# Performance work log

Hardware: AMD Instinct MI355X
Metric: run time of the kernel (lower is better)

Reference implementation:

```python
import jax, jax.numpy as jnp
import numpy as np

N, E, H, NH = 50000, 800000, 128, 4
D = H // NH
EPS = 1e-5


def _ln(x, g, b):
    m = jnp.mean(x, axis=-1, keepdims=True)
    v = jnp.mean((x - m) ** 2, axis=-1, keepdims=True)
    return (x - m) * jax.lax.rsqrt(v + EPS) * g + b


def setup_inputs() -> dict:
    key = jax.random.key(0)
    ks = jax.random.split(key, 16)

    def lin(k, fi, fo):
        w = jax.random.normal(k, (fi, fo), jnp.float32) * (1.0 / np.sqrt(fi))
        return w, jnp.zeros((fo,), jnp.float32)

    h = jax.random.normal(ks[0], (N, H), jnp.float32)
    e = jax.random.normal(ks[1], (E, H), jnp.float32)
    src = jax.random.randint(ks[2], (E,), 0, N, jnp.int32)
    dst = jax.random.randint(ks[3], (E,), 0, N, jnp.int32)

    Wq, bq = lin(ks[4], H, H)
    Wk, bk = lin(ks[5], 2 * H, H)
    Wv, bv = lin(ks[6], 2 * H, H)
    Wn1, bn1 = lin(ks[7], H, H)
    Wn2, bn2 = lin(ks[8], H, H)
    We1, be1 = lin(ks[9], 3 * H, H)
    We2, be2 = lin(ks[10], H, H)
    gh = jnp.ones((H,), jnp.float32)
    bh = jnp.zeros((H,), jnp.float32)
    ge = jnp.ones((H,), jnp.float32)
    be = jnp.zeros((H,), jnp.float32)

    return dict(h=h, e=e, src=src, dst=dst, Wq=Wq, bq=bq, Wk=Wk, bk=bk,
                Wv=Wv, bv=bv, Wn1=Wn1, bn1=bn1, Wn2=Wn2, bn2=bn2,
                We1=We1, be1=be1, We2=We2, be2=be2, gh=gh, bh=bh, ge=ge, be=be)


def reference(h, e, src, dst, Wq, bq, Wk, bk, Wv, bv, Wn1, bn1, Wn2, bn2,
              We1, be1, We2, be2, gh, bh, ge, be):
    # gather src node features onto edges, concat with edge features: [E, 2H]
    m = jnp.concatenate([h[src], e], axis=-1)
    Q = (h @ Wq + bq).reshape(N, NH, D)
    K = (m @ Wk + bk).reshape(E, NH, D)
    V = (m @ Wv + bv).reshape(E, NH, D)

    # per-edge multihead attention score against destination query: [E, NH]
    s = jnp.sum(Q[dst] * K, axis=-1) / np.sqrt(D).astype(np.float32)

    # destination-grouped (segment) softmax per head
    smax = jax.ops.segment_max(s, dst, num_segments=N)  # [N, NH]
    a = jnp.exp(s - smax[dst])
    denom = jax.ops.segment_sum(a, dst, num_segments=N)  # [N, NH]
    a = a / denom[dst]

    # weighted scatter-sum of values back to destination nodes
    msg = V * a[..., None]  # [E, NH, D]
    h_agg = jax.ops.segment_sum(msg, dst, num_segments=N).reshape(N, H)

    # node MLP update (dropout = identity in eval) + residual + LayerNorm
    h_new = jax.nn.relu(jax.nn.relu(h_agg @ Wn1 + bn1) @ Wn2 + bn2)
    h_out = _ln(h + h_new, gh, bh)

    # edge MLP update on [src_h, dst_h, e] + residual + LayerNorm
    me = jnp.concatenate([h_out[src], h_out[dst], e], axis=-1)  # [E, 3H]
    e_new = jax.nn.relu(jax.nn.relu(me @ We1 + be1) @ We2 + be2)
    e_out = _ln(e + e_new, ge, be)
    return h_out, e_out
```

## Files before the change

### kernel.cpp

```cpp
#include <hip/hip_runtime.h>
#include <hip/hip_bf16.h>

#define NN 50000
#define EE 800000
#define HH 128

typedef __attribute__((ext_vector_type(8))) short bf16x8;
typedef __attribute__((ext_vector_type(4))) float f32x4;

__device__ inline unsigned short f2bf(float f) {
    union { float f; unsigned u; } v; v.f = f;
    unsigned r = v.u + 0x7FFF + ((v.u >> 16) & 1);
    return (unsigned short)(r >> 16);
}

__global__ __launch_bounds__(256) void hist_k(const int* __restrict__ dst, int* __restrict__ cnt) {
    int i = blockIdx.x * 256 + threadIdx.x;
    if (i < EE) atomicAdd(&cnt[dst[i]], 1);
}

__global__ __launch_bounds__(256) void blocksum_k(const int* __restrict__ cnt, int* __restrict__ bsum) {
    __shared__ int sm[256];
    int i = blockIdx.x * 256 + threadIdx.x;
    sm[threadIdx.x] = (i < NN) ? cnt[i] : 0;
    __syncthreads();
    for (int s = 128; s > 0; s >>= 1) {
        if (threadIdx.x < s) sm[threadIdx.x] += sm[threadIdx.x + s];
        __syncthreads();
    }
    if (threadIdx.x == 0) bsum[blockIdx.x] = sm[0];
}

__global__ __launch_bounds__(256) void scanb_k(int* __restrict__ bsum, int nb) {
    __shared__ int sm[256];
    int t = threadIdx.x;
    sm[t] = (t < nb) ? bsum[t] : 0;
    __syncthreads();
    for (int d = 1; d < 256; d <<= 1) {
        int v = (t >= d) ? sm[t - d] : 0;
        __syncthreads();
        sm[t] += v;
        __syncthreads();
    }
    if (t < nb) bsum[t] = sm[t];
}

__global__ __launch_bounds__(256) void offsets_k(const int* __restrict__ cnt, const int* __restrict__ bsum,
                                                 int* __restrict__ offsets, int* __restrict__ cursor) {
    __shared__ int sm[256];
    int b = blockIdx.x, t = threadIdx.x;
    int i = b * 256 + t;
    int c = (i < NN) ? cnt[i] : 0;
    sm[t] = c;
    __syncthreads();
    for (int d = 1; d < 256; d <<= 1) {
        int v = (t >= d) ? sm[t - d] : 0;
        __syncthreads();
        sm[t] += v;
        __syncthreads();
    }
    int incl = sm[t];
    int base = (b == 0) ? 0 : bsum[b - 1];
    int off = base + incl - c;
    if (i < NN) { offsets[i] = off; cursor[i] = off; }
    if (i == NN - 1) offsets[NN] = off + c;
}

__global__ __launch_bounds__(256) void fill_k(const int* __restrict__ dst, int* __restrict__ cursor,
                                              int* __restrict__ eids) {
    int i = blockIdx.x * 256 + threadIdx.x;
    if (i < EE) { int p = atomicAdd(&cursor[dst[i]], 1); eids[p] = i; }
}

__global__ __launch_bounds__(256) void wprep_k(const float* __restrict__ W, unsigned short* __restrict__ out,
                                               int fi, int fo, int n_off, int out_ld) {
    int i = blockIdx.x * 256 + threadIdx.x;
    if (i >= fi * fo) return;
    int n = i / fi, k = i - n * fi;
    out[(size_t)(n_off + n) * out_ld + k] = f2bf(W[(size_t)k * fo + n]);
}

__global__ __launch_bounds__(256) void cvt_k(const float* __restrict__ in, unsigned short* __restrict__ out,
                                             long n8) {
    long i = (long)blockIdx.x * 256 + threadIdx.x;
    if (i >= n8) return;
    const float4* p = (const float4*)in + i * 2;
    float4 a = p[0], b = p[1];
    bf16x8 o = {(short)f2bf(a.x), (short)f2bf(a.y), (short)f2bf(a.z), (short)f2bf(a.w),
                (short)f2bf(b.x), (short)f2bf(b.y), (short)f2bf(b.z), (short)f2bf(b.w)};
    *((bf16x8*)out + i) = o;
}

template <int G, int NCW, int RT, int MODE>
__global__ __launch_bounds__(512, 2) void mm4_k(
    const unsigned short* __restrict__ A0, const int* __restrict__ idx0,
    const unsigned short* __restrict__ A1, const int* __restrict__ idx1,
    const unsigned short* __restrict__ A2, const int* __restrict__ idx2,
    const unsigned short* __restrict__ Wt, const float* __restrict__ bias,
    int M,
    float* __restrict__ Cf, unsigned short* __restrict__ Cb, int out_ld)
{
    constexpr int RW = 8 / NCW;
    constexpr int ROWS = RW * RT * 16;
    constexpr int Ktot = G * 128;
    constexpr int SI = ROWS / 32;
    __shared__ unsigned short Asl[G * ROWS * 128];

    const int t = threadIdx.x;
    const int wid = t >> 6, lane = t & 63;
    const int lr = lane & 15, lk = lane >> 4;
    const int colw = (NCW == 8) ? wid : (wid & 3);
    const int roww = (NCW == 8) ? 0 : (wid >> 2);
    const int col0 = colw << 5;
    const int tbase = blockIdx.x * ROWS;

    const unsigned short* As[3] = {A0, A1, A2};
    const int* igs[3] = {idx0, idx1, idx2};

    #pragma unroll
    for (int g = 0; g < G; ++g) {
        const unsigned short* Ag = As[g];
        const int* ig = igs[g];
        #pragma unroll
        for (int i = 0; i < SI; ++i) {
            int rl = ((i * 8 + wid) << 2) + (lane >> 4);
            int gr = tbase + rl; if (gr >= M) gr = M - 1;
            int rid = ig ? ig[gr] : gr;
            const unsigned short* src = Ag + (size_t)rid * HH + (((lane & 15) ^ (rl & 7)) << 3);
            unsigned short* dst = &Asl[(g * ROWS + ((i * 8 + wid) << 2)) << 7];
            __builtin_amdgcn_global_load_lds((const __attribute__((address_space(1))) void*)src,
                                             (__attribute__((address_space(3))) void*)dst, 16, 0, 0);
        }
    }

    f32x4 acc[RT][2];
    #pragma unroll
    for (int tt = 0; tt < RT; ++tt) { acc[tt][0] = (f32x4){0,0,0,0}; acc[tt][1] = (f32x4){0,0,0,0}; }

    __syncthreads();

    #pragma unroll
    for (int g = 0; g < G; ++g) {
        bf16x8 b[4][2];
        #pragma unroll
        for (int s = 0; s < 4; ++s)
            #pragma unroll
            for (int c = 0; c < 2; ++c)
                b[s][c] = *(const bf16x8*)(Wt + (size_t)(col0 + (c << 4) + lr) * Ktot + (g << 7) + (s << 5) + (lk << 3));

        #pragma unroll
        for (int tt = 0; tt < RT; ++tt) {
            const int tl = (tt * RW + roww) << 4;
            bf16x8 a[4];
            #pragma unroll
            for (int s = 0; s < 4; ++s) {
                const int c16 = ((s << 2) + lk) ^ (lr & 7);
                a[s] = *(const bf16x8*)&Asl[((g * ROWS + tl + lr) << 7) + (c16 << 3)];
            }
            #pragma unroll
            for (int s = 0; s < 4; ++s) {
                acc[tt][0] = __builtin_amdgcn_mfma_f32_16x16x32_bf16(a[s], b[s][0], acc[tt][0], 0, 0, 0);
                acc[tt][1] = __builtin_amdgcn_mfma_f32_16x16x32_bf16(a[s], b[s][1], acc[tt][1], 0, 0, 0);
            }
        }
    }

    float bias2[2] = {bias[col0 + lr], bias[col0 + 16 + lr]};
    #pragma unroll
    for (int tt = 0; tt < RT; ++tt) {
        #pragma unroll
        for (int rr = 0; rr < 4; ++rr) {
            int row = tbase + ((tt * RW + roww) << 4) + (lk << 2) + rr;
            if (row >= M) continue;
            #pragma unroll
            for (int c = 0; c < 2; ++c) {
                float v = acc[tt][c][rr] + bias2[c];
                if (MODE == 1 || MODE == 4) v = fmaxf(v, 0.f);
                size_t o = (size_t)row * out_ld + col0 + (c << 4) + lr;
                if (MODE == 0 || MODE == 1) Cf[o] = v;
                else Cb[o] = f2bf(v);
            }
        }
    }
}

template <int G, int RT>
__global__ __launch_bounds__(512, 2) void mlp_k(
    const unsigned short* __restrict__ A0, const int* __restrict__ idx0,
    const unsigned short* __restrict__ A1, const int* __restrict__ idx1,
    const unsigned short* __restrict__ A2, const int* __restrict__ idx2,
    const unsigned short* __restrict__ W1t, const float* __restrict__ b1,
    const unsigned short* __restrict__ W2t, const float* __restrict__ b2,
    int M,
    float* __restrict__ Cf, unsigned short* __restrict__ Cb2,
    const float* __restrict__ resid, const float* __restrict__ gamma, const float* __restrict__ beta)
{
    constexpr int RW = 2, NCW = 4;
    constexpr int ROWS = RW * RT * 16;
    constexpr int K1 = G * 128;
    constexpr int SI = ROWS / 32;
    __shared__ unsigned short Asl[G * ROWS * 128];
    __shared__ float lnbuf[RT * 32 * 8];

    const int t = threadIdx.x;
    const int wid = t >> 6, lane = t & 63;
    const int lr = lane & 15, lk = lane >> 4;
    const int colw = wid & 3, roww = wid >> 2;
    const int col0 = colw << 5;
    const int tbase = blockIdx.x * ROWS;

    const unsigned short* As[3] = {A0, A1, A2};
    const int* igs[3] = {idx0, idx1, idx2};

    #pragma unroll
    for (int g = 0; g < G; ++g) {
        const unsigned short* Ag = As[g];
        const int* ig = igs[g];
        #pragma unroll
        for (int i = 0; i < SI; ++i) {
            int rl = ((i * 8 + wid) << 2) + (lane >> 4);
            int gr = tbase + rl; if (gr >= M) gr = M - 1;
            int rid = ig ? ig[gr] : gr;
            const unsigned short* src = Ag + (size_t)rid * HH + (((lane & 15) ^ (rl & 7)) << 3);
            unsigned short* dst = &Asl[(g * ROWS + ((i * 8 + wid) << 2)) << 7];
            __builtin_amdgcn_global_load_lds((const __attribute__((address_space(1))) void*)src,
                                             (__attribute__((address_space(3))) void*)dst, 16, 0, 0);
        }
    }

    f32x4 acc[RT][2];
    #pragma unroll
    for (int tt = 0; tt < RT; ++tt) { acc[tt][0] = (f32x4){0,0,0,0}; acc[tt][1] = (f32x4){0,0,0,0}; }

    __syncthreads();

    #pragma unroll
    for (int g = 0; g < G; ++g) {
        bf16x8 b[4][2];
        #pragma unroll
        for (int s = 0; s < 4; ++s)
            #pragma unroll
            for (int c = 0; c < 2; ++c)
                b[s][c] = *(const bf16x8*)(W1t + (size_t)(col0 + (c << 4) + lr) * K1 + (g << 7) + (s << 5) + (lk << 3));

        #pragma unroll
        for (int tt = 0; tt < RT; ++tt) {
            const int tl = (tt * RW + roww) << 4;
            bf16x8 a[4];
            #pragma unroll
            for (int s = 0; s < 4; ++s) {
                const int c16 = ((s << 2) + lk) ^ (lr & 7);
                a[s] = *(const bf16x8*)&Asl[((g * ROWS + tl + lr) << 7) + (c16 << 3)];
            }
            #pragma unroll
            for (int s = 0; s < 4; ++s) {
                acc[tt][0] = __builtin_amdgcn_mfma_f32_16x16x32_bf16(a[s], b[s][0], acc[tt][0], 0, 0, 0);
                acc[tt][1] = __builtin_amdgcn_mfma_f32_16x16x32_bf16(a[s], b[s][1], acc[tt][1], 0, 0, 0);
            }
        }
    }

    __syncthreads();

    {
        float b1c[2] = {b1[col0 + lr], b1[col0 + 16 + lr]};
        #pragma unroll
        for (int tt = 0; tt < RT; ++tt) {
            #pragma unroll
            for (int rr = 0; rr < 4; ++rr) {
                int rowl = ((tt * RW + roww) << 4) + (lk << 2) + rr;
                #pragma unroll
                for (int c = 0; c < 2; ++c) {
                    int col = col0 + (c << 4) + lr;
                    int chunk = (col >> 3) ^ (rowl & 7);
                    Asl[(rowl << 7) + (chunk << 3) + (col & 7)] =
                        f2bf(fmaxf(acc[tt][c][rr] + b1c[c], 0.f));
                }
            }
        }
    }

    __syncthreads();

    f32x4 acc2[RT][2];
    #pragma unroll
    for (int tt = 0; tt < RT; ++tt) { acc2[tt][0] = (f32x4){0,0,0,0}; acc2[tt][1] = (f32x4){0,0,0,0}; }

    {
        bf16x8 b[4][2];
        #pragma unroll
        for (int s = 0; s < 4; ++s)
            #pragma unroll
            for (int c = 0; c < 2; ++c)
                b[s][c] = *(const bf16x8*)(W2t + (size_t)(col0 + (c << 4) + lr) * 128 + (s << 5) + (lk << 3));

        #pragma unroll
        for (int tt = 0; tt < RT; ++tt) {
            const int tl = (tt * RW + roww) << 4;
            bf16x8 a[4];
            #pragma unroll
            for (int s = 0; s < 4; ++s) {
                const int c16 = ((s << 2) + lk) ^ (lr & 7);
                a[s] = *(const bf16x8*)&Asl[((tl + lr) << 7) + (c16 << 3)];
            }
            #pragma unroll
            for (int s = 0; s < 4; ++s) {
                acc2[tt][0] = __builtin_amdgcn_mfma_f32_16x16x32_bf16(a[s], b[s][0], acc2[tt][0], 0, 0, 0);
                acc2[tt][1] = __builtin_amdgcn_mfma_f32_16x16x32_bf16(a[s], b[s][1], acc2[tt][1], 0, 0, 0);
            }
        }
    }

    float b2c[2] = {b2[col0 + lr], b2[col0 + 16 + lr]};
    float g2[2] = {gamma[col0 + lr], gamma[col0 + 16 + lr]};
    float be2[2] = {beta[col0 + lr], beta[col0 + 16 + lr]};

    #pragma unroll
    for (int tt = 0; tt < RT; ++tt) {
        #pragma unroll
        for (int rr = 0; rr < 4; ++rr) {
            int row = tbase + ((tt * RW + roww) << 4) + (lk << 2) + rr;
            int rowc = (row < M) ? row : M - 1;
            float sum = 0.f, sq = 0.f;
            #pragma unroll
            for (int c = 0; c < 2; ++c) {
                float v = fmaxf(acc2[tt][c][rr] + b2c[c], 0.f);
                v += resid[(size_t)rowc * HH + col0 + (c << 4) + lr];
                acc2[tt][c][rr] = v;
                sum += v; sq += v * v;
            }
            sum += __shfl_xor(sum, 1); sq += __shfl_xor(sq, 1);
            sum += __shfl_xor(sum, 2); sq += __shfl_xor(sq, 2);
            sum += __shfl_xor(sum, 4); sq += __shfl_xor(sq, 4);
            sum += __shfl_xor(sum, 8); sq += __shfl_xor(sq, 8);
            if (lr == 0) {
                int rls = (roww << 4) + (lk << 2) + rr;
                lnbuf[((tt * 32 + rls) << 3) + (colw << 1) + 0] = sum;
                lnbuf[((tt * 32 + rls) << 3) + (colw << 1) + 1] = sq;
            }
        }
    }
    __syncthreads();
    #pragma unroll
    for (int tt = 0; tt < RT; ++tt) {
        #pragma unroll
        for (int rr = 0; rr < 4; ++rr) {
            int rls = (roww << 4) + (lk << 2) + rr;
            float s4 = 0.f, q4 = 0.f;
            #pragma unroll
            for (int cw = 0; cw < 4; ++cw) {
                s4 += lnbuf[((tt * 32 + rls) << 3) + (cw << 1) + 0];
                q4 += lnbuf[((tt * 32 + rls) << 3) + (cw << 1) + 1];
            }
            const float mean = s4 * (1.f / 128.f);
            const float var = q4 * (1.f / 128.f) - mean * mean;
            const float rs = rsqrtf(var + 1e-5f);
            int row = tbase + ((tt * RW + roww) << 4) + (lk << 2) + rr;
            if (row < M) {
                #pragma unroll
                for (int c = 0; c < 2; ++c) {
                    float o = (acc2[tt][c][rr] - mean) * rs * g2[c] + be2[c];
                    size_t idx = (size_t)row * HH + col0 + (c << 4) + lr;
                    Cf[idx] = o;
                    if (Cb2) Cb2[idx] = f2bf(o);
                }
            }
        }
    }
}

template <int RT>
__global__ __launch_bounds__(512, 2) void kv_k(
    const unsigned short* __restrict__ hbf, const int* __restrict__ src,
    const unsigned short* __restrict__ ebf,
    const unsigned short* __restrict__ Wt, const float* __restrict__ bias,
    const float* __restrict__ Q, const int* __restrict__ dst,
    int M, unsigned short* __restrict__ V, float* __restrict__ sbuf)
{
    constexpr int ROWS = RT * 16;
    constexpr int Ktot = 256;
    constexpr int SI = ROWS / 32;
    __shared__ unsigned short Asl[2 * ROWS * 128];

    const int t = threadIdx.x;
    const int wid = t >> 6, lane = t & 63;
    const int lr = lane & 15, lk = lane >> 4;
    const int col0 = wid << 5;
    const int tbase = blockIdx.x * ROWS;

    int dstid[RT][4];
    if (wid < 4) {
        #pragma unroll
        for (int tt = 0; tt < RT; ++tt)
            #pragma unroll
            for (int rr = 0; rr < 4; ++rr) {
                int row = tbase + (tt << 4) + (lk << 2) + rr;
                dstid[tt][rr] = dst[(row < M) ? row : M - 1];
            }
    }

    #pragma unroll
    for (int g = 0; g < 2; ++g) {
        const unsigned short* Ag = g ? ebf : hbf;
        #pragma unroll
        for (int i = 0; i < SI; ++i) {
            int rl = ((i * 8 + wid) << 2) + (lane >> 4);
            int gr = tbase + rl; if (gr >= M) gr = M - 1;
            int rid = g ? gr : src[gr];
            const unsigned short* srcp = Ag + (size_t)rid * HH + (((lane & 15) ^ (rl & 7)) << 3);
            unsigned short* dstp = &Asl[(g * ROWS + ((i * 8 + wid) << 2)) << 7];
            __builtin_amdgcn_global_load_lds((const __attribute__((address_space(1))) void*)srcp,
                                             (__attribute__((address_space(3))) void*)dstp, 16, 0, 0);
        }
    }

    f32x4 acc[RT][2];
    #pragma unroll
    for (int tt = 0; tt < RT; ++tt) { acc[tt][0] = (f32x4){0,0,0,0}; acc[tt][1] = (f32x4){0,0,0,0}; }

    __syncthreads();

    #pragma unroll
    for (int g = 0; g < 2; ++g) {
        bf16x8 b[4][2];
        #pragma unroll
        for (int s = 0; s < 4; ++s)
            #pragma unroll
            for (int c = 0; c < 2; ++c)
                b[s][c] = *(const bf16x8*)(Wt + (size_t)(col0 + (c << 4) + lr) * Ktot + (g << 7) + (s << 5) + (lk << 3));

        #pragma unroll
        for (int tt = 0; tt < RT; ++tt) {
            bf16x8 a[4];
            #pragma unroll
            for (int s = 0; s < 4; ++s) {
                const int c16 = ((s << 2) + lk) ^ (lr & 7);
                a[s] = *(const bf16x8*)&Asl[((g * ROWS + (tt << 4) + lr) << 7) + (c16 << 3)];
            }
            #pragma unroll
            for (int s = 0; s < 4; ++s) {
                acc[tt][0] = __builtin_amdgcn_mfma_f32_16x16x32_bf16(a[s], b[s][0], acc[tt][0], 0, 0, 0);
                acc[tt][1] = __builtin_amdgcn_mfma_f32_16x16x32_bf16(a[s], b[s][1], acc[tt][1], 0, 0, 0);
            }
        }
    }

    float bias2[2] = {bias[col0 + lr], bias[col0 + 16 + lr]};

    if (wid < 4) {
        #pragma unroll
        for (int tt = 0; tt < RT; ++tt) {
            #pragma unroll
            for (int rr = 0; rr < 4; ++rr) {
                int row = tbase + (tt << 4) + (lk << 2) + rr;
                int d = dstid[tt][rr];
                float q0 = Q[(size_t)d * HH + col0 + lr];
                float q1 = Q[(size_t)d * HH + col0 + 16 + lr];
                float p = (acc[tt][0][rr] + bias2[0]) * q0 + (acc[tt][1][rr] + bias2[1]) * q1;
                p += __shfl_xor(p, 1); p += __shfl_xor(p, 2);
                p += __shfl_xor(p, 4); p += __shfl_xor(p, 8);
                if (lr == 0 && row < M)
                    sbuf[(size_t)row * 4 + wid] = p * 0.17677669529663687f;
            }
        }
    } else {
        #pragma unroll
        for (int tt = 0; tt < RT; ++tt) {
            #pragma unroll
            for (int rr = 0; rr < 4; ++rr) {
                int row = tbase + (tt << 4) + (lk << 2) + rr;
                if (row >= M) continue;
                #pragma unroll
                for (int c = 0; c < 2; ++c)
                    V[(size_t)row * HH + (col0 - 128) + (c << 4) + lr] = f2bf(acc[tt][c][rr] + bias2[c]);
            }
        }
    }
}

__global__ __launch_bounds__(256) void agg_k(const __hip_bfloat16* __restrict__ Vb,
                                             const float* __restrict__ s,
                                             const int* __restrict__ offsets,
                                             const int* __restrict__ eids,
                                             unsigned short* __restrict__ hagg)
{
    const int t = threadIdx.x;
    const int n = blockIdx.x * 4 + (t >> 6);
    if (n >= NN) return;
    const int lane = t & 63;
    const int c0 = lane, c1 = lane + 64;
    const int h0 = lane >> 5, h1 = h0 + 2;
    const int o0 = offsets[n], o1 = offsets[n + 1];
    float m0 = -1e30f, m1 = -1e30f, d0 = 0.f, d1 = 0.f, a0 = 0.f, a1 = 0.f;
    for (int j = o0; j < o1; ++j) {
        const int e = eids[j];
        const float s0 = s[(size_t)e * 4 + h0];
        const float s1 = s[(size_t)e * 4 + h1];
        const float v0 = __bfloat162float(Vb[(size_t)e * HH + c0]);
        const float v1 = __bfloat162float(Vb[(size_t)e * HH + c1]);
        float nm = fmaxf(m0, s0);
        float sc = __expf(m0 - nm);
        float w  = __expf(s0 - nm);
        d0 = d0 * sc + w; a0 = a0 * sc + w * v0; m0 = nm;
        nm = fmaxf(m1, s1);
        sc = __expf(m1 - nm);
        w  = __expf(s1 - nm);
        d1 = d1 * sc + w; a1 = a1 * sc + w * v1; m1 = nm;
    }
    const bool any = (o1 > o0);
    hagg[(size_t)n * HH + c0] = any ? f2bf(a0 / d0) : 0;
    hagg[(size_t)n * HH + c1] = any ? f2bf(a1 / d1) : 0;
}

extern "C" void kernel_launch(void* const* d_in, const int* in_sizes, int n_in,
                              void* d_out, int out_size, void* d_ws, size_t ws_size,
                              hipStream_t stream)
{
    const float* h   = (const float*)d_in[0];
    const float* e   = (const float*)d_in[1];
    const int*   src = (const int*)d_in[2];
    const int*   dst = (const int*)d_in[3];
    const float* Wq  = (const float*)d_in[4];
    const float* bq  = (const float*)d_in[5];
    const float* Wk  = (const float*)d_in[6];
    const float* bk  = (const float*)d_in[7];
    const float* Wv  = (const float*)d_in[8];
    const float* bv  = (const float*)d_in[9];
    const float* Wn1 = (const float*)d_in[10];
    const float* bn1 = (const float*)d_in[11];
    const float* Wn2 = (const float*)d_in[12];
    const float* bn2 = (const float*)d_in[13];
    const float* We1 = (const float*)d_in[14];
    const float* be1 = (const float*)d_in[15];
    const float* We2 = (const float*)d_in[16];
    const float* be2 = (const float*)d_in[17];
    const float* gh  = (const float*)d_in[18];
    const float* bh  = (const float*)d_in[19];
    const float* ge  = (const float*)d_in[20];
    const float* be_ = (const float*)d_in[21];
    (void)in_sizes; (void)n_in; (void)out_size; (void)ws_size;

    float* h_out = (float*)d_out;
    float* e_out = (float*)d_out + (size_t)NN * HH;

    char* ws = (char*)d_ws;
    size_t off = 0;
    auto carve = [&](size_t bytes) { void* p = ws + off; off += (bytes + 255) & ~(size_t)255; return p; };
    unsigned short* Vbuf = (unsigned short*)carve((size_t)EE * HH * 2);
    unsigned short* ebf = (unsigned short*)carve((size_t)EE * HH * 2);
    float* Q      = (float*)carve((size_t)NN * HH * 4);
    float* sbuf   = (float*)carve((size_t)EE * 4 * 4);
    unsigned short* hagg = (unsigned short*)carve((size_t)NN * HH * 2);
    unsigned short* hobf = (unsigned short*)carve((size_t)NN * HH * 2);
    unsigned short* hbf  = (unsigned short*)carve((size_t)NN * HH * 2);
    int* cursor   = (int*)carve((size_t)NN * 4);
    int* offsets  = (int*)carve((size_t)(NN + 1) * 4);
    int* bsum     = (int*)carve(256 * 4);
    int* eids     = (int*)carve((size_t)EE * 4);
    unsigned short* Wq_s  = (unsigned short*)carve(128 * 128 * 2);
    unsigned short* Wkv_s = (unsigned short*)carve(256 * 256 * 2);
    unsigned short* Wn1_s = (unsigned short*)carve(128 * 128 * 2);
    unsigned short* Wn2_s = (unsigned short*)carve(128 * 128 * 2);
    unsigned short* We1_s = (unsigned short*)carve(128 * 384 * 2);
    unsigned short* We2_s = (unsigned short*)carve(128 * 128 * 2);
    float* b_kv   = (float*)carve(256 * 4);

    const int nb = (NN + 255) / 256;

    wprep_k<<<(128 * 128 + 255) / 256, 256, 0, stream>>>(Wq,  Wq_s,  128, 128, 0, 128);
    wprep_k<<<(256 * 128 + 255) / 256, 256, 0, stream>>>(Wk,  Wkv_s, 256, 128, 0, 256);
    wprep_k<<<(256 * 128 + 255) / 256, 256, 0, stream>>>(Wv,  Wkv_s, 256, 128, 128, 256);
    wprep_k<<<(128 * 128 + 255) / 256, 256, 0, stream>>>(Wn1, Wn1_s, 128, 128, 0, 128);
    wprep_k<<<(128 * 128 + 255) / 256, 256, 0, stream>>>(Wn2, Wn2_s, 128, 128, 0, 128);
    wprep_k<<<(384 * 128 + 255) / 256, 256, 0, stream>>>(We1, We1_s, 384, 128, 0, 384);
    wprep_k<<<(128 * 128 + 255) / 256, 256, 0, stream>>>(We2, We2_s, 128, 128, 0, 128);
    hipMemcpyAsync(b_kv,       bk, 128 * 4, hipMemcpyDeviceToDevice, stream);
    hipMemcpyAsync(b_kv + 128, bv, 128 * 4, hipMemcpyDeviceToDevice, stream);

    cvt_k<<<(NN * HH / 8 + 255) / 256, 256, 0, stream>>>(h, hbf, (long)NN * HH / 8);
    cvt_k<<<(EE * HH / 8 + 255) / 256, 256, 0, stream>>>(e, ebf, (long)EE * HH / 8);

    hipMemsetAsync(cursor, 0, (size_t)NN * 4, stream);
    hist_k<<<(EE + 255) / 256, 256, 0, stream>>>(dst, cursor);
    blocksum_k<<<nb, 256, 0, stream>>>(cursor, bsum);
    scanb_k<<<1, 256, 0, stream>>>(bsum, nb);
    offsets_k<<<nb, 256, 0, stream>>>(cursor, bsum, offsets, cursor);
    fill_k<<<(EE + 255) / 256, 256, 0, stream>>>(dst, cursor, eids);

    mm4_k<1, 4, 4, 0><<<(NN + 127) / 128, 512, 0, stream>>>(
        hbf, nullptr, nullptr, nullptr, nullptr, nullptr,
        Wq_s, bq, NN, Q, nullptr, 128);

    kv_k<4><<<EE / 64, 512, 0, stream>>>(
        hbf, src, ebf, Wkv_s, b_kv, Q, dst, EE, Vbuf, sbuf);

    agg_k<<<(NN + 3) / 4, 256, 0, stream>>>((const __hip_bfloat16*)Vbuf, sbuf, offsets, eids, hagg);

    mlp_k<1, 4><<<(NN + 127) / 128, 512, 0, stream>>>(
        hagg, nullptr, nullptr, nullptr, nullptr, nullptr,
        Wn1_s, bn1, Wn2_s, bn2, NN, h_out, hobf, h, gh, bh);

    mlp_k<3, 2><<<EE / 64, 512, 0, stream>>>(
        hobf, src, hobf, dst, ebf, nullptr,
        We1_s, be1, We2_s, be2, EE, e_out, nullptr, e, ge, be_);
}
```

Baseline: 1.340 ms.

## Use 256-thread 32-row tiles for KV and MLP kernels, prefetch residual

```diff
diff --git a/kernel.cpp b/kernel.cpp
--- a/kernel.cpp
+++ b/kernel.cpp
@@ -94,8 +94,6 @@
 template <int G, int NCW, int RT, int MODE>
 __global__ __launch_bounds__(512, 2) void mm4_k(
     const unsigned short* __restrict__ A0, const int* __restrict__ idx0,
-    const unsigned short* __restrict__ A1, const int* __restrict__ idx1,
-    const unsigned short* __restrict__ A2, const int* __restrict__ idx2,
     const unsigned short* __restrict__ Wt, const float* __restrict__ bias,
     int M,
     float* __restrict__ Cf, unsigned short* __restrict__ Cb, int out_ld)
@@ -109,24 +107,19 @@
     const int t = threadIdx.x;
     const int wid = t >> 6, lane = t & 63;
     const int lr = lane & 15, lk = lane >> 4;
-    const int colw = (NCW == 8) ? wid : (wid & 3);
-    const int roww = (NCW == 8) ? 0 : (wid >> 2);
+    const int colw = wid & 3;
+    const int roww = wid >> 2;
     const int col0 = colw << 5;
     const int tbase = blockIdx.x * ROWS;
 
-    const unsigned short* As[3] = {A0, A1, A2};
-    const int* igs[3] = {idx0, idx1, idx2};
-
     #pragma unroll
     for (int g = 0; g < G; ++g) {
-        const unsigned short* Ag = As[g];
-        const int* ig = igs[g];
         #pragma unroll
         for (int i = 0; i < SI; ++i) {
             int rl = ((i * 8 + wid) << 2) + (lane >> 4);
             int gr = tbase + rl; if (gr >= M) gr = M - 1;
-            int rid = ig ? ig[gr] : gr;
-            const unsigned short* src = Ag + (size_t)rid * HH + (((lane & 15) ^ (rl & 7)) << 3);
+            int rid = idx0 ? idx0[gr] : gr;
+            const unsigned short* src = A0 + (size_t)rid * HH + (((lane & 15) ^ (rl & 7)) << 3);
             unsigned short* dst = &Asl[(g * ROWS + ((i * 8 + wid) << 2)) << 7];
             __builtin_amdgcn_global_load_lds((const __attribute__((address_space(1))) void*)src,
                                              (__attribute__((address_space(3))) void*)dst, 16, 0, 0);
@@ -175,7 +168,7 @@
             #pragma unroll
             for (int c = 0; c < 2; ++c) {
                 float v = acc[tt][c][rr] + bias2[c];
-                if (MODE == 1 || MODE == 4) v = fmaxf(v, 0.f);
+                if (MODE == 1) v = fmaxf(v, 0.f);
                 size_t o = (size_t)row * out_ld + col0 + (c << 4) + lr;
                 if (MODE == 0 || MODE == 1) Cf[o] = v;
                 else Cb[o] = f2bf(v);
@@ -184,8 +177,8 @@
     }
 }
 
-template <int G, int RT>
-__global__ __launch_bounds__(512, 2) void mlp_k(
+template <int G>
+__global__ __launch_bounds__(256, 4) void mlp4_k(
     const unsigned short* __restrict__ A0, const int* __restrict__ idx0,
     const unsigned short* __restrict__ A1, const int* __restrict__ idx1,
     const unsigned short* __restrict__ A2, const int* __restrict__ idx2,
@@ -195,34 +188,44 @@
     float* __restrict__ Cf, unsigned short* __restrict__ Cb2,
     const float* __restrict__ resid, const float* __restrict__ gamma, const float* __restrict__ beta)
 {
-    constexpr int RW = 2, NCW = 4;
-    constexpr int ROWS = RW * RT * 16;
+    constexpr int RT = 2;
+    constexpr int ROWS = RT * 16;
     constexpr int K1 = G * 128;
-    constexpr int SI = ROWS / 32;
     __shared__ unsigned short Asl[G * ROWS * 128];
-    __shared__ float lnbuf[RT * 32 * 8];
+    __shared__ float lnbuf[RT * 16 * 8];
 
     const int t = threadIdx.x;
     const int wid = t >> 6, lane = t & 63;
     const int lr = lane & 15, lk = lane >> 4;
-    const int colw = wid & 3, roww = wid >> 2;
-    const int col0 = colw << 5;
+    const int col0 = wid << 5;
     const int tbase = blockIdx.x * ROWS;
 
     const unsigned short* As[3] = {A0, A1, A2};
     const int* igs[3] = {idx0, idx1, idx2};
+
+    float rp[RT][4][2];
+    #pragma unroll
+    for (int tt = 0; tt < RT; ++tt)
+        #pragma unroll
+        for (int rr = 0; rr < 4; ++rr) {
+            int row = tbase + (tt << 4) + (lk << 2) + rr;
+            int rowc = (row < M) ? row : M - 1;
+            #pragma unroll
+            for (int c = 0; c < 2; ++c)
+                rp[tt][rr][c] = resid[(size_t)rowc * HH + col0 + (c << 4) + lr];
+        }
 
     #pragma unroll
     for (int g = 0; g < G; ++g) {
         const unsigned short* Ag = As[g];
         const int* ig = igs[g];
         #pragma unroll
-        for (int i = 0; i < SI; ++i) {
-            int rl = ((i * 8 + wid) << 2) + (lane >> 4);
+        for (int i = 0; i < 2; ++i) {
+            int rl = ((i * 4 + wid) << 2) + (lane >> 4);
             int gr = tbase + rl; if (gr >= M) gr = M - 1;
             int rid = ig ? ig[gr] : gr;
             const unsigned short* src = Ag + (size_t)rid * HH + (((lane & 15) ^ (rl & 7)) << 3);
-            unsigned short* dst = &Asl[(g * ROWS + ((i * 8 + wid) << 2)) << 7];
+            unsigned short* dst = &Asl[(g * ROWS + ((i * 4 + wid) << 2)) << 7];
             __builtin_amdgcn_global_load_lds((const __attribute__((address_space(1))) void*)src,
                                              (__attribute__((address_space(3))) void*)dst, 16, 0, 0);
         }
@@ -245,12 +248,11 @@
 
         #pragma unroll
         for (int tt = 0; tt < RT; ++tt) {
-            const int tl = (tt * RW + roww) << 4;
             bf16x8 a[4];
             #pragma unroll
             for (int s = 0; s < 4; ++s) {
                 const int c16 = ((s << 2) + lk) ^ (lr & 7);
-                a[s] = *(const bf16x8*)&Asl[((g * ROWS + tl + lr) << 7) + (c16 << 3)];
+                a[s] = *(const bf16x8*)&Asl[((g * ROWS + (tt << 4) + lr) << 7) + (c16 << 3)];
             }
             #pragma unroll
             for (int s = 0; s < 4; ++s) {
@@ -268,7 +270,7 @@
         for (int tt = 0; tt < RT; ++tt) {
             #pragma unroll
             for (int rr = 0; rr < 4; ++rr) {
-                int rowl = ((tt * RW + roww) << 4) + (lk << 2) + rr;
+                int rowl = (tt << 4) + (lk << 2) + rr;
                 #pragma unroll
                 for (int c = 0; c < 2; ++c) {
                     int col = col0 + (c << 4) + lr;
@@ -296,12 +298,11 @@
 
         #pragma unroll
         for (int tt = 0; tt < RT; ++tt) {
-            const int tl = (tt * RW + roww) << 4;
             bf16x8 a[4];
             #pragma unroll
             for (int s = 0; s < 4; ++s) {
                 const int c16 = ((s << 2) + lk) ^ (lr & 7);
-                a[s] = *(const bf16x8*)&Asl[((tl + lr) << 7) + (c16 << 3)];
+                a[s] = *(const bf16x8*)&Asl[(((tt << 4) + lr) << 7) + (c16 << 3)];
             }
             #pragma unroll
             for (int s = 0; s < 4; ++s) {
@@ -319,13 +320,10 @@
     for (int tt = 0; tt < RT; ++tt) {
         #pragma unroll
         for (int rr = 0; rr < 4; ++rr) {
-            int row = tbase + ((tt * RW + roww) << 4) + (lk << 2) + rr;
-            int rowc = (row < M) ? row : M - 1;
             float sum = 0.f, sq = 0.f;
             #pragma unroll
             for (int c = 0; c < 2; ++c) {
-                float v = fmaxf(acc2[tt][c][rr] + b2c[c], 0.f);
-                v += resid[(size_t)rowc * HH + col0 + (c << 4) + lr];
+                float v = fmaxf(acc2[tt][c][rr] + b2c[c], 0.f) + rp[tt][rr][c];
                 acc2[tt][c][rr] = v;
                 sum += v; sq += v * v;
             }
@@ -334,9 +332,9 @@
             sum += __shfl_xor(sum, 4); sq += __shfl_xor(sq, 4);
             sum += __shfl_xor(sum, 8); sq += __shfl_xor(sq, 8);
             if (lr == 0) {
-                int rls = (roww << 4) + (lk << 2) + rr;
-                lnbuf[((tt * 32 + rls) << 3) + (colw << 1) + 0] = sum;
-                lnbuf[((tt * 32 + rls) << 3) + (colw << 1) + 1] = sq;
+                int rls = (lk << 2) + rr;
+                lnbuf[((tt * 16 + rls) << 3) + (wid << 1) + 0] = sum;
+                lnbuf[((tt * 16 + rls) << 3) + (wid << 1) + 1] = sq;
             }
         }
     }
@@ -345,17 +343,17 @@
     for (int tt = 0; tt < RT; ++tt) {
         #pragma unroll
         for (int rr = 0; rr < 4; ++rr) {
-            int rls = (roww << 4) + (lk << 2) + rr;
+            int rls = (lk << 2) + rr;
             float s4 = 0.f, q4 = 0.f;
             #pragma unroll
             for (int cw = 0; cw < 4; ++cw) {
-                s4 += lnbuf[((tt * 32 + rls) << 3) + (cw << 1) + 0];
-                q4 += lnbuf[((tt * 32 + rls) << 3) + (cw << 1) + 1];
+                s4 += lnbuf[((tt * 16 + rls) << 3) + (cw << 1) + 0];
+                q4 += lnbuf[((tt * 16 + rls) << 3) + (cw << 1) + 1];
             }
             const float mean = s4 * (1.f / 128.f);
             const float var = q4 * (1.f / 128.f) - mean * mean;
             const float rs = rsqrtf(var + 1e-5f);
-            int row = tbase + ((tt * RW + roww) << 4) + (lk << 2) + rr;
+            int row = tbase + (tt << 4) + (lk << 2) + rr;
             if (row < M) {
                 #pragma unroll
                 for (int c = 0; c < 2; ++c) {
@@ -369,27 +367,25 @@
     }
 }
 
-template <int RT>
-__global__ __launch_bounds__(512, 2) void kv_k(
+__global__ __launch_bounds__(256, 4) void kv4_k(
     const unsigned short* __restrict__ hbf, const int* __restrict__ src,
     const unsigned short* __restrict__ ebf,
     const unsigned short* __restrict__ Wt, const float* __restrict__ bias,
     const float* __restrict__ Q, const int* __restrict__ dst,
     int M, unsigned short* __restrict__ V, float* __restrict__ sbuf)
 {
+    constexpr int RT = 2;
     constexpr int ROWS = RT * 16;
-    constexpr int Ktot = 256;
-    constexpr int SI = ROWS / 32;
     __shared__ unsigned short Asl[2 * ROWS * 128];
 
     const int t = threadIdx.x;
     const int wid = t >> 6, lane = t & 63;
     const int lr = lane & 15, lk = lane >> 4;
-    const int col0 = wid << 5;
+    const int col0 = wid << 6;
     const int tbase = blockIdx.x * ROWS;
 
     int dstid[RT][4];
-    if (wid < 4) {
+    if (wid < 2) {
         #pragma unroll
         for (int tt = 0; tt < RT; ++tt)
             #pragma unroll
@@ -403,51 +399,49 @@
     for (int g = 0; g < 2; ++g) {
         const unsigned short* Ag = g ? ebf : hbf;
         #pragma unroll
-        for (int i = 0; i < SI; ++i) {
-            int rl = ((i * 8 + wid) << 2) + (lane >> 4);
+        for (int i = 0; i < 2; ++i) {
+            int rl = ((i * 4 + wid) << 2) + (lane >> 4);
             int gr = tbase + rl; if (gr >= M) gr = M - 1;
             int rid = g ? gr : src[gr];
             const unsigned short* srcp = Ag + (size_t)rid * HH + (((lane & 15) ^ (rl & 7)) << 3);
-            unsigned short* dstp = &Asl[(g * ROWS + ((i * 8 + wid) << 2)) << 7];
+            unsigned short* dstp = &Asl[(g * ROWS + ((i * 4 + wid) << 2)) << 7];
             __builtin_amdgcn_global_load_lds((const __attribute__((address_space(1))) void*)srcp,
                                              (__attribute__((address_space(3))) void*)dstp, 16, 0, 0);
         }
     }
 
-    f32x4 acc[RT][2];
-    #pragma unroll
-    for (int tt = 0; tt < RT; ++tt) { acc[tt][0] = (f32x4){0,0,0,0}; acc[tt][1] = (f32x4){0,0,0,0}; }
+    f32x4 acc[RT][4];
+    #pragma unroll
+    for (int tt = 0; tt < RT; ++tt)
+        #pragma unroll
+        for (int c = 0; c < 4; ++c) acc[tt][c] = (f32x4){0,0,0,0};
 
     __syncthreads();
 
     #pragma unroll
     for (int g = 0; g < 2; ++g) {
-        bf16x8 b[4][2];
-        #pragma unroll
-        for (int s = 0; s < 4; ++s)
-            #pragma unroll
-            for (int c = 0; c < 2; ++c)
-                b[s][c] = *(const bf16x8*)(Wt + (size_t)(col0 + (c << 4) + lr) * Ktot + (g << 7) + (s << 5) + (lk << 3));
-
-        #pragma unroll
-        for (int tt = 0; tt < RT; ++tt) {
-            bf16x8 a[4];
-            #pragma unroll
-            for (int s = 0; s < 4; ++s) {
+        #pragma unroll
+        for (int s = 0; s < 4; ++s) {
+            bf16x8 b4[4];
+            #pragma unroll
+            for (int c = 0; c < 4; ++c)
+                b4[c] = *(const bf16x8*)(Wt + (size_t)(col0 + (c << 4) + lr) * 256 + (g << 7) + (s << 5) + (lk << 3));
+            #pragma unroll
+            for (int tt = 0; tt < RT; ++tt) {
                 const int c16 = ((s << 2) + lk) ^ (lr & 7);
-                a[s] = *(const bf16x8*)&Asl[((g * ROWS + (tt << 4) + lr) << 7) + (c16 << 3)];
-            }
-            #pragma unroll
-            for (int s = 0; s < 4; ++s) {
-                acc[tt][0] = __builtin_amdgcn_mfma_f32_16x16x32_bf16(a[s], b[s][0], acc[tt][0], 0, 0, 0);
-                acc[tt][1] = __builtin_amdgcn_mfma_f32_16x16x32_bf16(a[s], b[s][1], acc[tt][1], 0, 0, 0);
-            }
-        }
-    }
-
-    float bias2[2] = {bias[col0 + lr], bias[col0 + 16 + lr]};
-
-    if (wid < 4) {
+                bf16x8 a = *(const bf16x8*)&Asl[((g * ROWS + (tt << 4) + lr) << 7) + (c16 << 3)];
+                #pragma unroll
+                for (int c = 0; c < 4; ++c)
+                    acc[tt][c] = __builtin_amdgcn_mfma_f32_16x16x32_bf16(a, b4[c], acc[tt][c], 0, 0, 0);
+            }
+        }
+    }
+
+    float bias4[4];
+    #pragma unroll
+    for (int c = 0; c < 4; ++c) bias4[c] = bias[col0 + (c << 4) + lr];
+
+    if (wid < 2) {
         #pragma unroll
         for (int tt = 0; tt < RT; ++tt) {
             #pragma unroll
@@ -456,11 +450,18 @@
                 int d = dstid[tt][rr];
                 float q0 = Q[(size_t)d * HH + col0 + lr];
                 float q1 = Q[(size_t)d * HH + col0 + 16 + lr];
-                float p = (acc[tt][0][rr] + bias2[0]) * q0 + (acc[tt][1][rr] + bias2[1]) * q1;
-                p += __shfl_xor(p, 1); p += __shfl_xor(p, 2);
-                p += __shfl_xor(p, 4); p += __shfl_xor(p, 8);
-                if (lr == 0 && row < M)
-                    sbuf[(size_t)row * 4 + wid] = p * 0.17677669529663687f;
+                float q2 = Q[(size_t)d * HH + col0 + 32 + lr];
+                float q3 = Q[(size_t)d * HH + col0 + 48 + lr];
+                float p0 = (acc[tt][0][rr] + bias4[0]) * q0 + (acc[tt][1][rr] + bias4[1]) * q1;
+                float p1 = (acc[tt][2][rr] + bias4[2]) * q2 + (acc[tt][3][rr] + bias4[3]) * q3;
+                p0 += __shfl_xor(p0, 1); p1 += __shfl_xor(p1, 1);
+                p0 += __shfl_xor(p0, 2); p1 += __shfl_xor(p1, 2);
+                p0 += __shfl_xor(p0, 4); p1 += __shfl_xor(p1, 4);
+                p0 += __shfl_xor(p0, 8); p1 += __shfl_xor(p1, 8);
+                if (lr == 0 && row < M) {
+                    sbuf[(size_t)row * 4 + wid * 2 + 0] = p0 * 0.17677669529663687f;
+                    sbuf[(size_t)row * 4 + wid * 2 + 1] = p1 * 0.17677669529663687f;
+                }
             }
         }
     } else {
@@ -471,8 +472,8 @@
                 int row = tbase + (tt << 4) + (lk << 2) + rr;
                 if (row >= M) continue;
                 #pragma unroll
-                for (int c = 0; c < 2; ++c)
-                    V[(size_t)row * HH + (col0 - 128) + (c << 4) + lr] = f2bf(acc[tt][c][rr] + bias2[c]);
+                for (int c = 0; c < 4; ++c)
+                    V[(size_t)row * HH + (col0 - 128) + (c << 4) + lr] = f2bf(acc[tt][c][rr] + bias4[c]);
             }
         }
     }
@@ -588,19 +589,18 @@
     fill_k<<<(EE + 255) / 256, 256, 0, stream>>>(dst, cursor, eids);
 
     mm4_k<1, 4, 4, 0><<<(NN + 127) / 128, 512, 0, stream>>>(
-        hbf, nullptr, nullptr, nullptr, nullptr, nullptr,
-        Wq_s, bq, NN, Q, nullptr, 128);
-
-    kv_k<4><<<EE / 64, 512, 0, stream>>>(
+        hbf, nullptr, Wq_s, bq, NN, Q, nullptr, 128);
+
+    kv4_k<<<EE / 32, 256, 0, stream>>>(
         hbf, src, ebf, Wkv_s, b_kv, Q, dst, EE, Vbuf, sbuf);
 
     agg_k<<<(NN + 3) / 4, 256, 0, stream>>>((const __hip_bfloat16*)Vbuf, sbuf, offsets, eids, hagg);
 
-    mlp_k<1, 4><<<(NN + 127) / 128, 512, 0, stream>>>(
+    mlp4_k<1><<<(NN + 31) / 32, 256, 0, stream>>>(
         hagg, nullptr, nullptr, nullptr, nullptr, nullptr,
         Wn1_s, bn1, Wn2_s, bn2, NN, h_out, hobf, h, gh, bh);
 
-    mlp_k<3, 2><<<EE / 64, 512, 0, stream>>>(
+    mlp4_k<3><<<EE / 32, 256, 0, stream>>>(
         hobf, src, hobf, dst, ebf, nullptr,
         We1_s, be1, We2_s, be2, EE, e_out, nullptr, e, ge, be_);
 }
```

Result: no change. 1.359 ms (+1.4%).
